# Performance work log

Hardware: AMD Instinct MI355X
Metric: run time of the kernel (lower is better)

## Reference

```python
import jax, jax.numpy as jnp
import numpy as np

G = 512          # graphs in batch
NPG = 128        # nodes per graph (equal-sized so decoder batches)
TEMP = 0.1       # SimilarityDecoder temperature


def setup_inputs() -> dict:
    key = jax.random.key(0)
    ks = jax.random.split(key, 10)
    N, D, K, H, T = G * NPG, 512, 1024, 128, 10
    return {
        "x": jax.random.normal(ks[0], (N, D), jnp.float32),
        "batch": jnp.repeat(jnp.arange(G, dtype=jnp.int64), NPG),
        "codebook_input": jax.random.normal(ks[1], (K, D), jnp.float32),
        "fc1_w": jax.random.normal(ks[2], (H, D), jnp.float32) * (1.0 / np.sqrt(D)),
        "fc1_b": jax.random.normal(ks[3], (H,), jnp.float32) * 0.01,
        "fc2_w": jax.random.normal(ks[4], (D, H), jnp.float32) * (1.0 / np.sqrt(H)),
        "fc2_b": jax.random.normal(ks[5], (D,), jnp.float32) * 0.01,
        "causal": jax.random.normal(ks[6], (K, K), jnp.float32),
        "cls_w": jax.random.normal(ks[7], (T, D), jnp.float32) * (1.0 / np.sqrt(D)),
        "cls_b": jax.random.normal(ks[8], (T,), jnp.float32) * 0.01,
    }


def _segment_mean(v, batch, num_segments):
    s = jax.ops.segment_sum(v, batch, num_segments=num_segments)
    cnt = jax.ops.segment_sum(jnp.ones((v.shape[0], 1), v.dtype), batch, num_segments=num_segments)
    return s / jnp.maximum(cnt, 1.0)


def _batched_adj(z):
    # SimilarityDecoder: per-graph sigmoid(norm_z @ norm_z.T / temp); graphs equal-sized -> [G, n, n]
    zg = z.reshape(G, NPG, -1)
    zn = zg / jnp.maximum(jnp.linalg.norm(zg, axis=-1, keepdims=True), 1e-12)
    return jax.nn.sigmoid(jnp.einsum("gnd,gmd->gnm", zn, zn) / TEMP)


def reference(x, batch, codebook_input, fc1_w, fc1_b, fc2_w, fc2_b, causal, cls_w, cls_b):
    K = causal.shape[0]
    I = jnp.eye(K, dtype=x.dtype)

    # ---- VectorQuantizer ----
    h = jax.nn.sigmoid(codebook_input @ fc1_w.T + fc1_b)
    codebook_transformed = h @ fc2_w.T + fc2_b                 # [K, D]
    causal_effect = causal * (1.0 - I) + I                     # off-diag causal + identity
    cs = jax.nn.sigmoid(codebook_transformed)
    causal_diag = causal * I
    causal_cb = causal_effect @ (causal_diag @ cs)             # [K, D]
    counter_matrix = causal * (1.0 - I)                        # DegreeLayer assumed: off-diagonal mask
    counter_cb = causal_effect @ (counter_matrix @ cs)         # [K, D]

    # ---- ClassLayer ----
    pooled_x = _segment_mean(x, batch, G)                      # [G, D]
    # squared euclidean distances x vs causal_cb -> argmin codebook index
    d2 = (jnp.sum(x * x, 1, keepdims=True)
          - 2.0 * (x @ causal_cb.T)
          + jnp.sum(causal_cb * causal_cb, 1))                 # [N, K]
    idx = jnp.argmin(d2, axis=1)                               # [N]
    causal_nodes = x + causal_cb[idx]
    counter_nodes = counter_cb[idx]
    z_nodes = codebook_transformed[idx]                        # [N, D]
    pooled_causal = _segment_mean(causal_nodes, batch, G)
    pooled_counter = _segment_mean(counter_nodes, batch, G)
    causal_pre = pooled_causal @ cls_w.T + cls_b
    counter_pre = pooled_counter @ cls_w.T + cls_b
    y_pre = pooled_x @ jax.lax.stop_gradient(cls_w).T + jax.lax.stop_gradient(cls_b)

    # ---- SimilarityDecoder ----
    A_ori = _batched_adj(x)                                    # [G, n, n]
    A_rec = _batched_adj(z_nodes)

    return (causal_pre, counter_pre, y_pre, A_ori, A_rec,
            z_nodes, x, causal_diag, counter_matrix, pooled_causal, pooled_x)
```

## Files before the change

kernel.cpp:

```cpp
#include <hip/hip_runtime.h>
#include <math.h>

#define NG   512
#define NPG  128
#define NN   65536
#define DD   512
#define KK   1024
#define HH   128
#define TT   10

#define RES_TAU 1.0f
#define RES_CAP 65536

typedef __attribute__((ext_vector_type(8))) short short8;
typedef __attribute__((ext_vector_type(4))) float float4v;

static const long OFF_CPRE = 0;
static const long OFF_KPRE = 5120;
static const long OFF_YPRE = 10240;
static const long OFF_AORI = 15360;
static const long OFF_AREC = OFF_AORI + 8388608L;
static const long OFF_Z    = OFF_AREC + 8388608L;
static const long OFF_X    = OFF_Z + 33554432L;
static const long OFF_CD   = OFF_X + 33554432L;
static const long OFF_CM   = OFF_CD + 1048576L;
static const long OFF_PC   = OFF_CM + 1048576L;
static const long OFF_PX   = OFF_PC + 262144L;

__device__ __forceinline__ float sigm_fast(float v) { return 1.0f / (1.0f + __expf(-v)); }
__device__ __forceinline__ float sigm_acc (float v) { return 1.0f / (1.0f + expf(-v)); }

__global__ void k_diagmask(const float* __restrict__ causal,
                           float* __restrict__ cd, float* __restrict__ cm,
                           float* __restrict__ dv) {
  int i = blockIdx.x * 256 + threadIdx.x;
  int r = i >> 10, c = i & 1023;
  float v = causal[i];
  bool diag = (r == c);
  cd[i] = diag ? v : 0.0f;
  cm[i] = diag ? 0.0f : v;
  if (diag) dv[r] = v;
}

__global__ void k_fc1(const float* __restrict__ cbi, const float* __restrict__ w,
                      const float* __restrict__ b, float* __restrict__ h) {
  int i = blockIdx.x * 256 + threadIdx.x;
  int k = i >> 7, j = i & 127;
  const float4* xr = (const float4*)(cbi + (long)k * DD);
  const float4* wr = (const float4*)(w + (long)j * DD);
  float s = b[j];
  for (int d = 0; d < DD / 4; d++) {
    float4 a = xr[d], bb = wr[d];
    s += a.x * bb.x + a.y * bb.y + a.z * bb.z + a.w * bb.w;
  }
  h[i] = sigm_acc(s);
}

__global__ void k_fc2(const float* __restrict__ h, const float* __restrict__ w,
                      const float* __restrict__ b, float* __restrict__ ct,
                      float* __restrict__ cs) {
  int i = blockIdx.x * 256 + threadIdx.x;
  int k = i >> 9, d = i & 511;
  const float4* hr = (const float4*)(h + (long)k * HH);
  const float4* wr = (const float4*)(w + (long)d * HH);
  float s = b[d];
  for (int j = 0; j < HH / 4; j++) {
    float4 a = hr[j], bb = wr[j];
    s += a.x * bb.x + a.y * bb.y + a.z * bb.z + a.w * bb.w;
  }
  ct[i] = s;
  cs[i] = sigm_acc(s);
}

template <int AM, int BM>
__launch_bounds__(256)
__global__ void gemm64(const float* __restrict__ A, const float* __restrict__ B,
                       const float* __restrict__ dscale, float* __restrict__ C,
                       int M, int Nc, int Kr) {
  __shared__ __align__(16) float as[32][68];
  __shared__ __align__(16) float bs[32][68];
  int tid = threadIdx.x;
  int tx = tid & 15, ty = tid >> 4;
  int m0 = blockIdx.y * 64, n0 = blockIdx.x * 64;
  float acc[4][4] = {};
  for (int kt = 0; kt < Kr; kt += 32) {
    for (int s = tid; s < 512; s += 256) {
      int m = s >> 3, c4 = (s & 7) << 2;
      int gr = m0 + m, gc = kt + c4;
      float4 v = *(const float4*)&A[(long)gr * Kr + gc];
      float vv[4] = {v.x, v.y, v.z, v.w};
      if (AM == 1) {
#pragma unroll
        for (int q = 0; q < 4; q++) if (gc + q == gr) vv[q] = 1.0f;
      } else if (AM == 2) {
#pragma unroll
        for (int q = 0; q < 4; q++) if (gc + q == gr) vv[q] = 0.0f;
      }
      as[c4 + 0][m] = vv[0]; as[c4 + 1][m] = vv[1];
      as[c4 + 2][m] = vv[2]; as[c4 + 3][m] = vv[3];
    }
    for (int s = tid; s < 512; s += 256) {
      int r = s >> 4, c4 = (s & 15) << 2;
      float4 v = *(const float4*)&B[(long)(kt + r) * Nc + n0 + c4];
      if (BM == 1) {
        float sc = dscale[kt + r];
        v.x *= sc; v.y *= sc; v.z *= sc; v.w *= sc;
      }
      *(float4*)&bs[r][c4] = v;
    }
    __syncthreads();
#pragma unroll
    for (int r = 0; r < 32; r++) {
      float4 a4 = *(const float4*)&as[r][ty * 4];
      float4 b4 = *(const float4*)&bs[r][tx * 4];
      float av[4] = {a4.x, a4.y, a4.z, a4.w};
      float bv[4] = {b4.x, b4.y, b4.z, b4.w};
#pragma unroll
      for (int i = 0; i < 4; i++)
#pragma unroll
        for (int j = 0; j < 4; j++) acc[i][j] += av[i] * bv[j];
    }
    __syncthreads();
  }
#pragma unroll
  for (int i = 0; i < 4; i++) {
    float4 v = make_float4(acc[i][0], acc[i][1], acc[i][2], acc[i][3]);
    *(float4*)&C[(long)(m0 + ty * 4 + i) * Nc + n0 + tx * 4] = v;
  }
}

__global__ void k_cnorm(const float* __restrict__ ccb, float* __restrict__ cn2,
                        int* __restrict__ rc) {
  if (blockIdx.x == 0 && threadIdx.x == 0) *rc = 0;
  int row = blockIdx.x * 4 + (threadIdx.x >> 6);
  int lane = threadIdx.x & 63;
  const float* r = ccb + (long)row * DD;
  float s = 0.0f;
  for (int q = 0; q < DD; q += 64) { float v = r[lane + q]; s += v * v; }
  for (int off = 32; off > 0; off >>= 1) s += __shfl_down(s, off);
  if (lane == 0) cn2[row] = s;
}

__device__ __forceinline__ ushort bf16_rne(float f, float* back) {
  unsigned int b = __float_as_uint(f);
  unsigned int r = b + 0x7fffu + ((b >> 16) & 1u);
  ushort h = (ushort)(r >> 16);
  *back = __uint_as_float(((unsigned int)h) << 16);
  return h;
}

__global__ void k_split(const float4* __restrict__ src, ushort* __restrict__ hi,
                        ushort* __restrict__ lo, long n4) {
  long i = (long)blockIdx.x * 256 + threadIdx.x;
  if (i >= n4) return;
  float4 v = src[i];
  float vv[4] = {v.x, v.y, v.z, v.w};
  ushort h[4], l[4];
#pragma unroll
  for (int q = 0; q < 4; q++) {
    float back;
    h[q] = bf16_rne(vv[q], &back);
    float rem = vv[q] - back;
    float dummy;
    l[q] = bf16_rne(rem, &dummy);
  }
  ((ushort4*)hi)[i] = make_ushort4(h[0], h[1], h[2], h[3]);
  ((ushort4*)lo)[i] = make_ushort4(l[0], l[1], l[2], l[3]);
}

__launch_bounds__(512, 2)
__global__ void k_argmin_mfma(const ushort* __restrict__ xh, const ushort* __restrict__ xl,
                              const ushort* __restrict__ ch, const ushort* __restrict__ cl,
                              const float* __restrict__ cn2, int* __restrict__ idxg,
                              int* __restrict__ rc, int* __restrict__ rlist) {
  __shared__ __align__(16) ushort xsh[64 * 512];
  __shared__ __align__(16) ushort xsl[64 * 512];
  __shared__ float cn2s[KK];
  __shared__ float mm1[8][64], mm2[8][64];
  __shared__ int   mid[8][64];

  int tid = threadIdx.x;
  long n0 = (long)blockIdx.x * 64;

  uint4 tmp[16];
#pragma unroll
  for (int r = 0; r < 16; r++) {
    int g = tid + r * 512;
    int rid = g >> 6;
    int node = rid & 63;
    int gb = (g & 63) << 4;
    const ushort* src = ((rid < 64) ? xh : xl) + (n0 + node) * (long)DD;
    tmp[r] = *(const uint4*)((const char*)src + gb);
  }
  for (int s = tid; s < KK; s += 512) cn2s[s] = cn2[s];
#pragma unroll
  for (int r = 0; r < 16; r++) {
    int g = tid + r * 512;
    int rid = g >> 6;
    int node = rid & 63;
    int gb = (g & 63) << 4;
    int db = gb ^ ((node & 7) << 4);
    ushort* dst = (rid < 64) ? xsh : xsl;
    *(uint4*)((char*)dst + node * 1024 + db) = tmp[r];
  }
  __syncthreads();

  int lane = tid & 63, wave = tid >> 6;
  int col = lane & 15, quad = lane >> 4;

  float m1[16], m2[16]; int id1[16];
#pragma unroll
  for (int s = 0; s < 16; s++) { m1[s] = 3.4e38f; m2[s] = 3.4e38f; id1[s] = 0; }

  const float4v vzero = {0.0f, 0.0f, 0.0f, 0.0f};
  float4v acc[4][4];

  for (int cc = 0; cc < 2; cc++) {
    int cb0 = cc * 512 + wave * 64;
#pragma unroll
    for (int i = 0; i < 4; i++)
#pragma unroll
      for (int j = 0; j < 4; j++) acc[i][j] = vzero;

    for (int dt = 0; dt < DD; dt += 32) {
      short8 bh[4], bl[4];
#pragma unroll
      for (int j = 0; j < 4; j++) {
        long crow = (long)(cb0 + j * 16 + col);
        const ushort* cph = ch + crow * DD + dt + quad * 8;
        const ushort* cpl = cl + crow * DD + dt + quad * 8;
        bh[j] = *(const short8*)cph;
        bl[j] = *(const short8*)cpl;
      }
      short8 ah[4], al[4];
#pragma unroll
      for (int i = 0; i < 4; i++) {
        int node = i * 16 + col;
        int db = (dt * 2 + quad * 16) ^ ((node & 7) << 4);
        ah[i] = *(const short8*)((const char*)xsh + node * 1024 + db);
        al[i] = *(const short8*)((const char*)xsl + node * 1024 + db);
      }
#pragma unroll
      for (int j = 0; j < 4; j++) {
#pragma unroll
        for (int i = 0; i < 4; i++) {
          acc[i][j] = __builtin_amdgcn_mfma_f32_16x16x32_bf16(ah[i], bh[j], acc[i][j], 0, 0, 0);
          acc[i][j] = __builtin_amdgcn_mfma_f32_16x16x32_bf16(ah[i], bl[j], acc[i][j], 0, 0, 0);
          acc[i][j] = __builtin_amdgcn_mfma_f32_16x16x32_bf16(al[i], bh[j], acc[i][j], 0, 0, 0);
        }
      }
    }
#pragma unroll
    for (int j = 0; j < 4; j++) {
      int code = cb0 + j * 16 + col;
      float c2 = cn2s[code];
#pragma unroll
      for (int i = 0; i < 4; i++) {
#pragma unroll
        for (int r = 0; r < 4; r++) {
          float v = fmaf(-2.0f, acc[i][j][r], c2);
          int s = i * 4 + r;
          if (v < m1[s] || (v == m1[s] && code < id1[s])) {
            m2[s] = m1[s]; m1[s] = v; id1[s] = code;
          } else if (v < m2[s]) {
            m2[s] = v;
          }
        }
      }
    }
  }
#pragma unroll
  for (int s = 0; s < 16; s++) {
#pragma unroll
    for (int mask = 1; mask <= 8; mask <<= 1) {
      float om1 = __shfl_xor(m1[s], mask);
      float om2 = __shfl_xor(m2[s], mask);
      int   oid = __shfl_xor(id1[s], mask);
      if (om1 < m1[s] || (om1 == m1[s] && oid < id1[s])) {
        m2[s] = fminf(m1[s], om2); m1[s] = om1; id1[s] = oid;
      } else {
        m2[s] = fminf(m2[s], om1);
      }
    }
  }
  if (col == 0) {
#pragma unroll
    for (int s = 0; s < 16; s++) {
      int i = s >> 2, r = s & 3;
      int nl = i * 16 + quad * 4 + r;
      mm1[wave][nl] = m1[s]; mm2[wave][nl] = m2[s]; mid[wave][nl] = id1[s];
    }
  }
  __syncthreads();
  if (tid < 64) {
    float f1 = mm1[0][tid], f2 = mm2[0][tid]; int fi = mid[0][tid];
#pragma unroll
    for (int w = 1; w < 8; w++) {
      float b1 = mm1[w][tid], b2 = mm2[w][tid]; int bi = mid[w][tid];
      if (b1 < f1 || (b1 == f1 && bi < fi)) {
        f2 = fminf(f1, b2); f1 = b1; fi = bi;
      } else {
        f2 = fminf(f2, b1);
      }
    }
    idxg[n0 + tid] = fi;
    if (f2 - f1 < RES_TAU) {
      int p = atomicAdd(rc, 1);
      if (p < RES_CAP) rlist[p] = (int)(n0 + tid);
    }
  }
}

__global__ void k_rescue(const float* __restrict__ x, const float* __restrict__ ccb,
                         const float* __restrict__ cn2, const int* __restrict__ rc,
                         const int* __restrict__ rlist, int* __restrict__ idxg) {
  __shared__ float xs[DD];
  __shared__ float bv[256]; __shared__ int bi[256];
  int count = *rc; if (count > RES_CAP) count = RES_CAP;
  int tid = threadIdx.x;
  for (int f = blockIdx.x; f < count; f += gridDim.x) {
    int n = rlist[f];
    for (int s = tid; s < DD; s += 256) xs[s] = x[(long)n * DD + s];
    __syncthreads();
    float best = 3.4e38f; int besti = 0;
    for (int c = tid; c < KK; c += 256) {
      const float4* cr = (const float4*)(ccb + (long)c * DD);
      const float4* xr = (const float4*)xs;
      float dot = 0.0f;
      for (int d = 0; d < DD / 4; d++) {
        float4 a = xr[d], b = cr[d];
        dot += a.x * b.x + a.y * b.y + a.z * b.z + a.w * b.w;
      }
      float v = cn2[c] - 2.0f * dot;
      if (v < best || (v == best && c < besti)) { best = v; besti = c; }
    }
    bv[tid] = best; bi[tid] = besti;
    __syncthreads();
    for (int off = 128; off > 0; off >>= 1) {
      if (tid < off) {
        float ov = bv[tid + off]; int oi = bi[tid + off];
        if (ov < bv[tid] || (ov == bv[tid] && oi < bi[tid])) { bv[tid] = ov; bi[tid] = oi; }
      }
      __syncthreads();
    }
    if (tid == 0) idxg[n] = bi[0];
    __syncthreads();
  }
}

__global__ void k_gather(const float4* __restrict__ ct4, const int* __restrict__ idxg,
                         float4* __restrict__ z4) {
  long i = (long)blockIdx.x * 256 + threadIdx.x;
  int n = (int)(i >> 7), c = (int)(i & 127);
  z4[i] = ct4[(long)idxg[n] * 128 + c];
}

__global__ void k_pool(const float* __restrict__ x, const float* __restrict__ ccb,
                       const float* __restrict__ kcb, const int* __restrict__ idxg,
                       float* __restrict__ px, float* __restrict__ pc,
                       float* __restrict__ pk) {
  __shared__ int sidx[NPG];
  int g = blockIdx.x, tid = threadIdx.x;
  if (tid < NPG) sidx[tid] = idxg[g * NPG + tid];
  __syncthreads();
  int d = tid;
  float sx = 0.0f, sc = 0.0f, sk = 0.0f;
  for (int n = 0; n < NPG; n++) {
    sx += x[((long)g * NPG + n) * DD + d];
    long r = (long)sidx[n] * DD + d;
    sc += ccb[r]; sk += kcb[r];
  }
  px[(long)g * DD + d] = sx / 128.0f;
  pc[(long)g * DD + d] = (sx + sc) / 128.0f;
  pk[(long)g * DD + d] = sk / 128.0f;
}

__global__ void k_heads(const float* __restrict__ pc, const float* __restrict__ pk,
                        const float* __restrict__ px, const float* __restrict__ w,
                        const float* __restrict__ b, float* __restrict__ cpre,
                        float* __restrict__ kpre, float* __restrict__ ypre) {
  int g = blockIdx.x, t = threadIdx.x;
  if (t >= 30) return;
  int which = t / 10, tt = t % 10;
  const float* src = (which == 0) ? pc : ((which == 1) ? pk : px);
  const float* sr = src + (long)g * DD;
  const float* wr = w + (long)tt * DD;
  float s = 0.0f;
  for (int d = 0; d < DD; d++) s += sr[d] * wr[d];
  s += b[tt];
  float* dst = (which == 0) ? cpre : ((which == 1) ? kpre : ypre);
  dst[g * TT + tt] = s;
}

__global__ void k_copy(const float4* __restrict__ src, float4* __restrict__ dst) {
  long i = (long)blockIdx.x * 256 + threadIdx.x;
  dst[i] = src[i];
}

__launch_bounds__(256)
__global__ void k_adj(const float* __restrict__ Z, float* __restrict__ Aout) {
  __shared__ float nrm[NPG];
  __shared__ float inv[NPG];
  __shared__ __align__(16) float zs[32][132];
  int tid = threadIdx.x;
  int g = blockIdx.x;
  const float* base = Z + (long)g * NPG * DD;
  if (tid < NPG) nrm[tid] = 0.0f;
  __syncthreads();
  for (int k = 0; k < 64; k++) {
    long i = (long)k * 256 + tid;
    int n = (int)(i >> 7);
    float4 v = ((const float4*)base)[i];
    float s = v.x * v.x + v.y * v.y + v.z * v.z + v.w * v.w;
    for (int off = 32; off > 0; off >>= 1) s += __shfl_down(s, off);
    if ((tid & 63) == 0) atomicAdd(&nrm[n], s);
  }
  __syncthreads();
  if (tid < NPG) inv[tid] = 1.0f / fmaxf(sqrtf(nrm[tid]), 1e-12f);
  __syncthreads();
  float acc[8][8] = {};
  int tx = tid & 15, ty = tid >> 4;
  for (int dt = 0; dt < DD; dt += 32) {
    for (int s = tid; s < 1024; s += 256) {
      int n = s >> 3, c4 = (s & 7) << 2;
      float4 v = *(const float4*)&base[(long)n * DD + dt + c4];
      float iv = inv[n];
      zs[c4 + 0][n] = v.x * iv; zs[c4 + 1][n] = v.y * iv;
      zs[c4 + 2][n] = v.z * iv; zs[c4 + 3][n] = v.w * iv;
    }
    __syncthreads();
#pragma unroll 8
    for (int r = 0; r < 32; r++) {
      float rv[8], cv[8];
      *(float4*)&rv[0] = *(const float4*)&zs[r][ty * 8];
      *(float4*)&rv[4] = *(const float4*)&zs[r][ty * 8 + 4];
      *(float4*)&cv[0] = *(const float4*)&zs[r][tx * 8];
      *(float4*)&cv[4] = *(const float4*)&zs[r][tx * 8 + 4];
#pragma unroll
      for (int i = 0; i < 8; i++)
#pragma unroll
        for (int j = 0; j < 8; j++) acc[i][j] += rv[i] * cv[j];
    }
    __syncthreads();
  }
  float* aout = Aout + (long)g * NPG * NPG;
#pragma unroll
  for (int i = 0; i < 8; i++) {
    int rr = ty * 8 + i;
    float o[8];
#pragma unroll
    for (int j = 0; j < 8; j++) o[j] = sigm_fast(acc[i][j] * 10.0f);
    *(float4*)&aout[(long)rr * NPG + tx * 8]     = make_float4(o[0], o[1], o[2], o[3]);
    *(float4*)&aout[(long)rr * NPG + tx * 8 + 4] = make_float4(o[4], o[5], o[6], o[7]);
  }
}

extern "C" void kernel_launch(void* const* d_in, const int* in_sizes, int n_in,
                              void* d_out, int out_size, void* d_ws, size_t ws_size,
                              hipStream_t stream) {
  const float* x      = (const float*)d_in[0];
  const float* cbi    = (const float*)d_in[2];
  const float* fc1w   = (const float*)d_in[3];
  const float* fc1b   = (const float*)d_in[4];
  const float* fc2w   = (const float*)d_in[5];
  const float* fc2b   = (const float*)d_in[6];
  const float* causal = (const float*)d_in[7];
  const float* clsw   = (const float*)d_in[8];
  const float* clsb   = (const float*)d_in[9];
  float* out = (float*)d_out;

  float* cpre = out + OFF_CPRE;
  float* kpre = out + OFF_KPRE;
  float* ypre = out + OFF_YPRE;

  float* scr  = out + OFF_AORI;
  float* h    = scr;
  float* cs   = scr + 131072L;
  float* tmp2 = scr + 655360L;
  float* ccb  = scr + 1179648L;
  float* kcb  = scr + 1703936L;
  float* cn2  = scr + 2228224L;
  int*   idxg = (int*)(scr + 2229248L);
  float* pk   = scr + 2294784L;
  float* dv   = scr + 2556928L;
  ushort* ch  = (ushort*)(scr + 2557952L);
  ushort* cl  = (ushort*)(scr + 2820096L);
  int*   rc   = (int*)(scr + 3082240L);
  int*   rlist= (int*)(scr + 3082496L);
  float* ct   = out + OFF_AREC;
  ushort* xh  = (ushort*)(out + OFF_X);
  ushort* xl  = (ushort*)(out + OFF_X + 16777216L);

  k_diagmask<<<4096, 256, 0, stream>>>(causal, out + OFF_CD, out + OFF_CM, dv);
  k_fc1<<<512, 256, 0, stream>>>(cbi, fc1w, fc1b, h);
  k_fc2<<<2048, 256, 0, stream>>>(h, fc2w, fc2b, ct, cs);
  gemm64<2, 0><<<dim3(8, 16), 256, 0, stream>>>(causal, cs,   nullptr, tmp2, KK, DD, KK);
  gemm64<1, 1><<<dim3(8, 16), 256, 0, stream>>>(causal, cs,   dv,      ccb,  KK, DD, KK);
  gemm64<1, 0><<<dim3(8, 16), 256, 0, stream>>>(causal, tmp2, nullptr, kcb,  KK, DD, KK);
  k_cnorm<<<256, 256, 0, stream>>>(ccb, cn2, rc);
  k_split<<<32768, 256, 0, stream>>>((const float4*)x, xh, xl, 8388608L);
  k_split<<<512, 256, 0, stream>>>((const float4*)ccb, ch, cl, 131072L);
  k_argmin_mfma<<<1024, 512, 0, stream>>>(xh, xl, ch, cl, cn2, idxg, rc, rlist);
  k_rescue<<<128, 256, 0, stream>>>(x, ccb, cn2, rc, rlist, idxg);
  k_gather<<<32768, 256, 0, stream>>>((const float4*)ct, idxg, (float4*)(out + OFF_Z));
  k_pool<<<512, 512, 0, stream>>>(x, ccb, kcb, idxg, out + OFF_PX, out + OFF_PC, pk);
  k_heads<<<512, 64, 0, stream>>>(out + OFF_PC, pk, out + OFF_PX, clsw, clsb, cpre, kpre, ypre);
  k_copy<<<32768, 256, 0, stream>>>((const float4*)x, (float4*)(out + OFF_X));
  k_adj<<<512, 256, 0, stream>>>(out + OFF_Z, out + OFF_AREC);
  k_adj<<<512, 256, 0, stream>>>(x, out + OFF_AORI);
}
```

Baseline: 1.767 ms.

## Double-buffer operand loads in codebook-distance MFMA loop with raised wave priority

Restructures the inner K loop of the nearest-codebook GEMM so that both operand sets are held in two register buffers. The next 32-wide slice (codebook rows from global memory, x rows from LDS) is fetched while MFMAs run on the current slice. Address bases are precomputed once, with an equivalent rewrite of the LDS XOR swizzle, and the MFMA burst is wrapped in s_setprio. The aim is to hide load latency behind matrix math, at the cost of extra VGPR pressure that may reduce occupancy.

```diff
diff --git a/kernel.cpp b/kernel.cpp
--- a/kernel.cpp
+++ b/kernel.cpp
@@ -208,48 +208,73 @@
   int lane = tid & 63, wave = tid >> 6;
   int col = lane & 15, quad = lane >> 4;
 
+  int abase[4];
+#pragma unroll
+  for (int i = 0; i < 4; i++) {
+    int node = i * 16 + col;
+    abase[i] = node * 1024 + ((quad ^ (node & 3)) << 4) + (((node >> 2) & 1) << 6);
+  }
+
+  const ushort* pBh[4];
+  const ushort* pBl[4];
+#pragma unroll
+  for (int j = 0; j < 4; j++) {
+    long row = (long)(wave * 64 + j * 16 + col);
+    pBh[j] = ch + row * DD + quad * 8;
+    pBl[j] = cl + row * DD + quad * 8;
+  }
+
   float m1[16], m2[16]; int id1[16];
 #pragma unroll
   for (int s = 0; s < 16; s++) { m1[s] = 3.4e38f; m2[s] = 3.4e38f; id1[s] = 0; }
 
   const float4v vzero = {0.0f, 0.0f, 0.0f, 0.0f};
   float4v acc[4][4];
+  short8 ahA[4], alA[4], bhA[4], blA[4];
+  short8 ahB[4], alB[4], bhB[4], blB[4];
+
+#define PREF(K, AH, AL, BH, BL)                                                  \
+  do {                                                                           \
+    int k_ = (K);                                                                \
+    _Pragma("unroll") for (int j = 0; j < 4; j++) {                              \
+      BH[j] = *(const short8*)(pBh[j] + k_ * 32);                                \
+      BL[j] = *(const short8*)(pBl[j] + k_ * 32);                                \
+    }                                                                            \
+    _Pragma("unroll") for (int i = 0; i < 4; i++) {                              \
+      int ao_ = abase[i] ^ (k_ << 6);                                            \
+      AH[i] = *(const short8*)((const char*)xsh + ao_);                          \
+      AL[i] = *(const short8*)((const char*)xsl + ao_);                          \
+    }                                                                            \
+  } while (0)
+
+#define COMP(AH, AL, BH, BL)                                                     \
+  do {                                                                           \
+    __builtin_amdgcn_s_setprio(1);                                               \
+    _Pragma("unroll") for (int j = 0; j < 4; j++)                                \
+      _Pragma("unroll") for (int i = 0; i < 4; i++) {                            \
+        acc[i][j] = __builtin_amdgcn_mfma_f32_16x16x32_bf16(AH[i], BH[j], acc[i][j], 0, 0, 0); \
+        acc[i][j] = __builtin_amdgcn_mfma_f32_16x16x32_bf16(AH[i], BL[j], acc[i][j], 0, 0, 0); \
+        acc[i][j] = __builtin_amdgcn_mfma_f32_16x16x32_bf16(AL[i], BH[j], acc[i][j], 0, 0, 0); \
+      }                                                                          \
+    __builtin_amdgcn_s_setprio(0);                                               \
+  } while (0)
 
   for (int cc = 0; cc < 2; cc++) {
+#pragma unroll
+    for (int i = 0; i < 4; i++)
+#pragma unroll
+      for (int j = 0; j < 4; j++) acc[i][j] = vzero;
+
+    PREF(0, ahA, alA, bhA, blA);
+#pragma unroll 1
+    for (int k = 0; k < 16; k += 2) {
+      PREF(k + 1, ahB, alB, bhB, blB);
+      COMP(ahA, alA, bhA, blA);
+      PREF((k + 2) & 15, ahA, alA, bhA, blA);
+      COMP(ahB, alB, bhB, blB);
+    }
+
     int cb0 = cc * 512 + wave * 64;
-#pragma unroll
-    for (int i = 0; i < 4; i++)
-#pragma unroll
-      for (int j = 0; j < 4; j++) acc[i][j] = vzero;
-
-    for (int dt = 0; dt < DD; dt += 32) {
-      short8 bh[4], bl[4];
-#pragma unroll
-      for (int j = 0; j < 4; j++) {
-        long crow = (long)(cb0 + j * 16 + col);
-        const ushort* cph = ch + crow * DD + dt + quad * 8;
-        const ushort* cpl = cl + crow * DD + dt + quad * 8;
-        bh[j] = *(const short8*)cph;
-        bl[j] = *(const short8*)cpl;
-      }
-      short8 ah[4], al[4];
-#pragma unroll
-      for (int i = 0; i < 4; i++) {
-        int node = i * 16 + col;
-        int db = (dt * 2 + quad * 16) ^ ((node & 7) << 4);
-        ah[i] = *(const short8*)((const char*)xsh + node * 1024 + db);
-        al[i] = *(const short8*)((const char*)xsl + node * 1024 + db);
-      }
-#pragma unroll
-      for (int j = 0; j < 4; j++) {
-#pragma unroll
-        for (int i = 0; i < 4; i++) {
-          acc[i][j] = __builtin_amdgcn_mfma_f32_16x16x32_bf16(ah[i], bh[j], acc[i][j], 0, 0, 0);
-          acc[i][j] = __builtin_amdgcn_mfma_f32_16x16x32_bf16(ah[i], bl[j], acc[i][j], 0, 0, 0);
-          acc[i][j] = __builtin_amdgcn_mfma_f32_16x16x32_bf16(al[i], bh[j], acc[i][j], 0, 0, 0);
-        }
-      }
-    }
 #pragma unroll
     for (int j = 0; j < 4; j++) {
       int code = cb0 + j * 16 + col;
@@ -268,7 +293,12 @@
         }
       }
     }
-  }
+#pragma unroll
+    for (int j = 0; j < 4; j++) { pBh[j] += 512 * DD; pBl[j] += 512 * DD; }
+  }
+#undef PREF
+#undef COMP
+
 #pragma unroll
   for (int s = 0; s < 16; s++) {
 #pragma unroll
```

Measured after the change: 1.745 ms. About the same (-1.3%).
